# Kernel tuning notes

Measured on AMD Instinct MI355X. Metric: run time of the kernel, lower is better.

## Reference

```python
import jax, jax.numpy as jnp
import numpy as np

N_USERS = 100000
N_ITEMS = 100000
N_NODES = N_USERS + N_ITEMS
NNZ = 3200000
EMB = 64
HOPS = 3


def setup_inputs() -> dict:
    key = jax.random.key(0)
    ks = jax.random.split(key, 9)
    return {
        "rows": jax.random.randint(ks[0], (NNZ,), 0, N_NODES, dtype=jnp.int32),
        "cols": jax.random.randint(ks[1], (NNZ,), 0, N_NODES, dtype=jnp.int32),
        "vals": jax.random.uniform(ks[2], (NNZ,), dtype=jnp.float32),
        "user_emb": jax.random.normal(ks[3], (N_USERS, EMB), dtype=jnp.float32) * 0.1,
        "item_emb": jax.random.normal(ks[4], (N_ITEMS, EMB), dtype=jnp.float32) * 0.1,
        "W_gc": jax.random.normal(ks[5], (HOPS, EMB, EMB), dtype=jnp.float32) * 0.1,
        "b_gc": jax.random.normal(ks[6], (HOPS, EMB), dtype=jnp.float32) * 0.1,
        "W_bi": jax.random.normal(ks[7], (HOPS, EMB, EMB), dtype=jnp.float32) * 0.1,
        "b_bi": jax.random.normal(ks[8], (HOPS, EMB), dtype=jnp.float32) * 0.1,
    }


def reference(rows, cols, vals, user_emb, item_emb, W_gc, b_gc, W_bi, b_bi):
    # NGCF.gcn with edge_dropout=False, mess_dropout=False.
    n_nodes = user_emb.shape[0] + item_emb.shape[0]
    ego = jnp.concatenate([user_emb, item_emb], axis=0)  # [N, d]
    all_embeddings = [ego]
    for k in range(W_gc.shape[0]):
        # sparse adjacency propagation: side = A_hat @ ego
        msgs = vals[:, None] * ego[cols]                       # [nnz, d]
        side = jax.ops.segment_sum(msgs, rows, num_segments=n_nodes)  # [N, d]
        sum_emb = side @ W_gc[k] + b_gc[k]                     # [N, d]
        bi_emb = (ego * side) @ W_bi[k] + b_bi[k]              # [N, d]
        ego = jax.nn.leaky_relu(sum_emb + bi_emb, negative_slope=0.2)
        nrm = jnp.sqrt(jnp.sum(ego * ego, axis=1, keepdims=True))
        all_embeddings.append(ego / jnp.maximum(nrm, 1e-12))   # F.normalize(p=2, dim=1)
    # [N, hops+1, d]; original splits into users/items — concatenated here
    return jnp.stack(all_embeddings, axis=1)
```

## Files before the change

kernel.cpp:

```cpp
#include <hip/hip_runtime.h>
#include <hip/hip_fp16.h>

#define N_USERS 100000
#define N_ITEMS 100000
#define N_NODES 200000
#define NNZ     3200000
#define EMB     64
#define HOPS    3
#define SLOTS   (HOPS + 1)
#define ROWSTRIDE (SLOTS * EMB)

#define BROWS 1024
#define NBUCK ((N_NODES + BROWS - 1) / BROWS)
#define CAPB  20
#define EPB   2048
#define TILE  64
#define LPAD  33


__global__ __launch_bounds__(256) void init_ego_q(
    const float* __restrict__ user_emb,
    const float* __restrict__ item_emb,
    float* __restrict__ out,
    signed char* __restrict__ ego8, float* __restrict__ esc)
{
    int gid = blockIdx.x * blockDim.x + threadIdx.x;
    int n = gid >> 6;
    int d = gid & 63;
    if (n >= N_NODES) return;
    float v = (n < N_USERS) ? user_emb[(size_t)n * EMB + d]
                            : item_emb[(size_t)(n - N_USERS) * EMB + d];
    out[(size_t)n * ROWSTRIDE + d] = v;

    float mx = fabsf(v);
    #pragma unroll
    for (int o = 32; o > 0; o >>= 1) mx = fmaxf(mx, __shfl_xor(mx, o));
    float inv = (mx > 0.f) ? 127.f / mx : 0.f;
    ego8[(size_t)n * EMB + d] = (signed char)__float2int_rn(v * inv);
    if (d == 0) esc[n] = mx * (1.f / 127.f);
}

__global__ __launch_bounds__(256) void hist_buckets(
    const int* __restrict__ rows, int* __restrict__ bcnt)
{
    __shared__ int h[NBUCK];
    int t = threadIdx.x;
    if (t < NBUCK) h[t] = 0;
    __syncthreads();
    for (int e = blockIdx.x * blockDim.x + t; e < NNZ; e += gridDim.x * blockDim.x)
        atomicAdd(&h[rows[e] >> 10], 1);
    __syncthreads();
    if (t < NBUCK && h[t]) atomicAdd(&bcnt[t], h[t]);
}

__global__ __launch_bounds__(256) void scan196(
    const int* __restrict__ bcnt, int* __restrict__ boff,
    int* __restrict__ gcur, int* __restrict__ off)
{
    __shared__ int sdata[256];
    int t = threadIdx.x;
    int v = (t < NBUCK) ? bcnt[t] : 0;
    sdata[t] = v;
    __syncthreads();
    #pragma unroll
    for (int ofs = 1; ofs < 256; ofs <<= 1) {
        int add = (t >= ofs) ? sdata[t - ofs] : 0;
        __syncthreads();
        sdata[t] += add;
        __syncthreads();
    }
    if (t < NBUCK) {
        int excl = sdata[t] - v;
        boff[t] = excl;
        gcur[t] = excl;
    }
    if (t == NBUCK - 1) boff[NBUCK] = sdata[t];
    if (t == 0) off[N_NODES] = NNZ;
}

__global__ __launch_bounds__(256) void bucketize(
    const int* __restrict__ rows, const int* __restrict__ cols,
    const float* __restrict__ vals,
    int* __restrict__ gcur,
    unsigned int* __restrict__ cvg, unsigned short* __restrict__ rlg)
{
    __shared__ int hist[NBUCK];
    __shared__ int lofs[NBUCK];
    __shared__ int cnt2[NBUCK];
    __shared__ int gbase[NBUCK];
    __shared__ int sscan[256];
    __shared__ unsigned int   stcv[EPB];
    __shared__ unsigned short strl[EPB];
    __shared__ int            sdst[EPB];

    int t = threadIdx.x;

    for (int base = blockIdx.x * EPB; base < NNZ; base += gridDim.x * EPB) {
        int e1 = min(base + EPB, NNZ);
        int cnt = e1 - base;

        if (t < NBUCK) { hist[t] = 0; cnt2[t] = 0; }
        __syncthreads();

        int myb[8];
        unsigned int mycv[8];
        unsigned short myrl[8];
        #pragma unroll
        for (int u = 0; u < 8; ++u) {
            int idx = base + u * 256 + t;
            myb[u] = -1;
            if (idx < e1) {
                int r = rows[idx];
                int c = cols[idx];
                float v = vals[idx];
                myb[u] = r >> 10;
                unsigned int q14 = (unsigned int)(v * 16383.f + 0.5f);
                mycv[u] = ((unsigned int)c << 14) | q14;
                myrl[u] = (unsigned short)(r & 1023);
                atomicAdd(&hist[myb[u]], 1);
            }
        }
        __syncthreads();

        int hv = (t < NBUCK) ? hist[t] : 0;
        sscan[t] = hv;
        __syncthreads();
        #pragma unroll
        for (int o = 1; o < 256; o <<= 1) {
            int add = (t >= o) ? sscan[t - o] : 0;
            __syncthreads();
            sscan[t] += add;
            __syncthreads();
        }
        if (t < NBUCK) {
            lofs[t] = sscan[t] - hv;
            gbase[t] = atomicAdd(&gcur[t], hv);
        }
        __syncthreads();

        #pragma unroll
        for (int u = 0; u < 8; ++u) {
            if (myb[u] >= 0) {
                int rank = atomicAdd(&cnt2[myb[u]], 1);
                int p = lofs[myb[u]] + rank;
                stcv[p] = mycv[u];
                strl[p] = myrl[u];
                sdst[p] = gbase[myb[u]] + rank;
            }
        }
        __syncthreads();

        for (int j = t; j < cnt; j += 256) {
            int dp = sdst[j];
            cvg[dp] = stcv[j];
            rlg[dp] = strl[j];
        }
        __syncthreads();
    }
}

__global__ __launch_bounds__(1024) void csr_bucket(
    const int* __restrict__ boff,
    unsigned int* __restrict__ cv, const unsigned short* __restrict__ rl,
    int* __restrict__ off)
{
    __shared__ int curL[BROWS];
    __shared__ int sWaveSum[16];
    __shared__ int sWaveOff[16];

    int b = blockIdx.x;
    int t = threadIdx.x;
    int s = boff[b];
    int e = boff[b + 1];

    unsigned int  ecv[CAPB];
    unsigned short erl[CAPB];
    #pragma unroll
    for (int i = 0; i < CAPB; ++i) {
        int idx = s + i * 1024 + t;
        if (idx < e) { ecv[i] = cv[idx]; erl[i] = rl[idx]; }
    }

    curL[t] = 0;
    __syncthreads();

    #pragma unroll
    for (int i = 0; i < CAPB; ++i) {
        int idx = s + i * 1024 + t;
        if (idx < e) atomicAdd(&curL[(int)erl[i]], 1);
    }
    __syncthreads();

    int lane = t & 63;
    int wid  = t >> 6;
    int v = curL[t];
    int inc = v;
    #pragma unroll
    for (int o = 1; o < 64; o <<= 1) {
        int up = __shfl_up(inc, o);
        if (lane >= o) inc += up;
    }
    if (lane == 63) sWaveSum[wid] = inc;
    __syncthreads();
    if (t < 16) {
        int w = sWaveSum[t];
        int wi = w;
        #pragma unroll
        for (int o = 1; o < 16; o <<= 1) {
            int up = __shfl_up(wi, o);
            if (t >= o) wi += up;
        }
        sWaveOff[t] = wi - w;
    }
    __syncthreads();
    int excl = inc - v + sWaveOff[wid];

    int row = b * BROWS + t;
    if (row < N_NODES) off[row] = s + excl;
    __syncthreads();
    curL[t] = s + excl;
    __syncthreads();

    #pragma unroll
    for (int i = 0; i < CAPB; ++i) {
        int idx = s + i * 1024 + t;
        if (idx < e) {
            int p = atomicAdd(&curL[(int)erl[i]], 1);
            cv[p] = ecv[i];
        }
    }
}

__global__ __launch_bounds__(256) void scale_edges(
    const uint4* __restrict__ cv4, const float* __restrict__ esc,
    ushort4* __restrict__ wn4)
{
    const float VS = 1.f / 16383.f;
    int i = blockIdx.x * blockDim.x + threadIdx.x;
    if (i >= NNZ / 4) return;
    uint4 c = cv4[i];
    ushort4 w;
    w.x = __half_as_ushort(__float2half((float)(c.x & 16383u) * VS * esc[c.x >> 14]));
    w.y = __half_as_ushort(__float2half((float)(c.y & 16383u) * VS * esc[c.y >> 14]));
    w.z = __half_as_ushort(__float2half((float)(c.z & 16383u) * VS * esc[c.z >> 14]));
    w.w = __half_as_ushort(__float2half((float)(c.w & 16383u) * VS * esc[c.w >> 14]));
    wn4[i] = w;
}

__device__ __forceinline__ void gstep4(
    const signed char* __restrict__ ego8,
    unsigned c0, unsigned c1, unsigned c2, unsigned c3,
    unsigned wlo, unsigned whi, unsigned g, unsigned dq,
    float& a0, float& a1, float& a2, float& a3)
{
    unsigned cs = (g & 2u) ? ((g & 1u) ? c3 : c2) : ((g & 1u) ? c1 : c0);
    unsigned wd = (g & 2u) ? whi : wlo;
    unsigned short wh = (g & 1u) ? (unsigned short)(wd >> 16)
                                 : (unsigned short)(wd & 0xFFFFu);
    float w = __half2float(__ushort_as_half(wh));
    uchar4 x4 = *(const uchar4*)(ego8 + (size_t)(cs >> 14) * EMB + dq * 4u);
    a0 = fmaf(w, (float)(signed char)x4.x, a0);
    a1 = fmaf(w, (float)(signed char)x4.y, a1);
    a2 = fmaf(w, (float)(signed char)x4.z, a2);
    a3 = fmaf(w, (float)(signed char)x4.w, a3);
}

__device__ __forceinline__ void gstepm(
    const signed char* __restrict__ ego8,
    const unsigned int* __restrict__ cv, const unsigned short* __restrict__ wn,
    int e, int hi, unsigned g, unsigned dq,
    float& a0, float& a1, float& a2, float& a3)
{
    int idx = e + (int)g;
    int cl = (idx < hi) ? idx : hi - 1;
    unsigned c = cv[cl];
    float w = (idx < hi) ? __half2float(__ushort_as_half(wn[cl])) : 0.f;
    uchar4 x4 = *(const uchar4*)(ego8 + (size_t)(c >> 14) * EMB + dq * 4u);
    a0 = fmaf(w, (float)(signed char)x4.x, a0);
    a1 = fmaf(w, (float)(signed char)x4.y, a1);
    a2 = fmaf(w, (float)(signed char)x4.z, a2);
    a3 = fmaf(w, (float)(signed char)x4.w, a3);
}

__global__ __launch_bounds__(256, 4) void gather_side(
    const int* __restrict__ off, const unsigned int* __restrict__ cv,
    const unsigned short* __restrict__ wn,
    const signed char* __restrict__ ego8,
    float* __restrict__ out, int k)
{
    int t = threadIdx.x;
    int lane = t & 63;
    unsigned g  = (unsigned)(lane >> 4);
    unsigned dq = (unsigned)(lane & 15);
    int gw = (int)((blockIdx.x * (size_t)blockDim.x + t) >> 6);
    int nw = (gridDim.x * blockDim.x) >> 6;

    float* dst = out + (size_t)(k + 1) * EMB;

    for (int n = gw; n < N_NODES; n += nw) {
        int beg = __builtin_amdgcn_readfirstlane(off[n]);
        int end = __builtin_amdgcn_readfirstlane(off[n + 1]);
        float a0 = 0.f, a1 = 0.f, a2 = 0.f, a3 = 0.f;
        int e = beg;
        if (e < end && (e & 3)) {
            int ea = (e + 3) & ~3;
            int ub = (ea < end) ? ea : end;
            gstepm(ego8, cv, wn, e, ub, g, dq, a0, a1, a2, a3);
            e = ea;
        }
        for (; e + 16 <= end; e += 16) {
            uint4 ca = *(const uint4*)(cv + e);
            uint4 cb = *(const uint4*)(cv + e + 4);
            uint4 cc = *(const uint4*)(cv + e + 8);
            uint4 cd = *(const uint4*)(cv + e + 12);
            uint2 w0 = *(const uint2*)(wn + e);
            uint2 w1 = *(const uint2*)(wn + e + 4);
            uint2 w2 = *(const uint2*)(wn + e + 8);
            uint2 w3 = *(const uint2*)(wn + e + 12);
            gstep4(ego8, ca.x, ca.y, ca.z, ca.w, w0.x, w0.y, g, dq, a0, a1, a2, a3);
            gstep4(ego8, cb.x, cb.y, cb.z, cb.w, w1.x, w1.y, g, dq, a0, a1, a2, a3);
            gstep4(ego8, cc.x, cc.y, cc.z, cc.w, w2.x, w2.y, g, dq, a0, a1, a2, a3);
            gstep4(ego8, cd.x, cd.y, cd.z, cd.w, w3.x, w3.y, g, dq, a0, a1, a2, a3);
        }
        for (; e < end; e += 4)
            gstepm(ego8, cv, wn, e, end, g, dq, a0, a1, a2, a3);

        a0 += __shfl_xor(a0, 16); a0 += __shfl_xor(a0, 32);
        a1 += __shfl_xor(a1, 16); a1 += __shfl_xor(a1, 32);
        a2 += __shfl_xor(a2, 16); a2 += __shfl_xor(a2, 32);
        a3 += __shfl_xor(a3, 16); a3 += __shfl_xor(a3, 32);
        if (g == 0) {
            float4 o4; o4.x = a0; o4.y = a1; o4.z = a2; o4.w = a3;
            *(float4*)(dst + (size_t)n * ROWSTRIDE + dq * 4u) = o4;
        }
    }
}

__global__ __launch_bounds__(256) void transform_v4(
    const float* __restrict__ Wg, const float* __restrict__ bg,
    const float* __restrict__ Wb, const float* __restrict__ bb,
    signed char* __restrict__ ego8, float* __restrict__ esc,
    float* __restrict__ out, int k, int writeNext)
{
    __shared__ float sS [TILE * LPAD];
    __shared__ float sES[TILE * LPAD];
    __shared__ float rsum[4][TILE];
    __shared__ float rmax[4][TILE];

    int t = threadIdx.x;
    int lane = t & 63;
    int dbase = __builtin_amdgcn_readfirstlane((t >> 6) * 16);

    float* slotK1 = out + (size_t)(k + 1) * EMB;
    int node0 = blockIdx.x * TILE;

    float acc[16];
    #pragma unroll
    for (int di = 0; di < 16; ++di) acc[di] = 0.f;

    int f4 = (t & 7) * 4;
    int nn = t >> 3;

    for (int p = 0; p < 2; ++p) {
        #pragma unroll
        for (int rep = 0; rep < 2; ++rep) {
            int n = nn + 32 * rep;
            size_t sbase = (size_t)(node0 + n) * ROWSTRIDE + 32 * p + f4;
            float4 s4 = *(const float4*)(slotK1 + sbase);
            uchar4 e4 = *(const uchar4*)(ego8 + (size_t)(node0 + n) * EMB + 32 * p + f4);
            float scn = esc[node0 + n];
            int lb = n * LPAD + f4;
            sS [lb + 0] = s4.x; sS [lb + 1] = s4.y; sS [lb + 2] = s4.z; sS [lb + 3] = s4.w;
            sES[lb + 0] = (float)(signed char)e4.x * scn * s4.x;
            sES[lb + 1] = (float)(signed char)e4.y * scn * s4.y;
            sES[lb + 2] = (float)(signed char)e4.z * scn * s4.z;
            sES[lb + 3] = (float)(signed char)e4.w * scn * s4.w;
        }
        __syncthreads();

        for (int jj = 0; jj < 32; ++jj) {
            float sv = sS [lane * LPAD + jj];
            float ev = sES[lane * LPAD + jj];
            int j = 32 * p + jj;
            const float* wgrow = Wg + j * EMB + dbase;
            const float* wbrow = Wb + j * EMB + dbase;
            #pragma unroll
            for (int di = 0; di < 16; ++di)
                acc[di] = fmaf(sv, wgrow[di], fmaf(ev, wbrow[di], acc[di]));
        }
        __syncthreads();
    }

    float o[16];
    float ps = 0.f, pm = 0.f;
    #pragma unroll
    for (int di = 0; di < 16; ++di) {
        float v = acc[di] + (bg[dbase + di] + bb[dbase + di]);
        v = (v > 0.f) ? v : 0.2f * v;
        o[di] = v;
        ps = fmaf(v, v, ps);
        pm = fmaxf(pm, fabsf(v));
    }
    int w = t >> 6;
    rsum[w][lane] = ps;
    rmax[w][lane] = pm;
    __syncthreads();
    float tot = rsum[0][lane] + rsum[1][lane] + rsum[2][lane] + rsum[3][lane];
    float mx  = fmaxf(fmaxf(rmax[0][lane], rmax[1][lane]),
                      fmaxf(rmax[2][lane], rmax[3][lane]));
    float scale = 1.f / fmaxf(sqrtf(tot), 1e-12f);

    if (writeNext) {
        float inv = (mx > 0.f) ? 127.f / mx : 0.f;
        unsigned int wd[4];
        #pragma unroll
        for (int q = 0; q < 4; ++q) {
            unsigned int b0 = (unsigned int)(unsigned char)(signed char)__float2int_rn(o[4*q+0] * inv);
            unsigned int b1 = (unsigned int)(unsigned char)(signed char)__float2int_rn(o[4*q+1] * inv);
            unsigned int b2 = (unsigned int)(unsigned char)(signed char)__float2int_rn(o[4*q+2] * inv);
            unsigned int b3 = (unsigned int)(unsigned char)(signed char)__float2int_rn(o[4*q+3] * inv);
            wd[q] = b0 | (b1 << 8) | (b2 << 16) | (b3 << 24);
        }
        uint4 pk; pk.x = wd[0]; pk.y = wd[1]; pk.z = wd[2]; pk.w = wd[3];
        *(uint4*)(ego8 + (size_t)(node0 + lane) * EMB + dbase) = pk;
        if (t < TILE) esc[node0 + lane] = mx * (1.f / 127.f);
    }

    float* dstp = slotK1 + (size_t)(node0 + lane) * ROWSTRIDE + dbase;
    #pragma unroll
    for (int q = 0; q < 4; ++q) {
        float4 o4;
        o4.x = o[4 * q + 0] * scale;
        o4.y = o[4 * q + 1] * scale;
        o4.z = o[4 * q + 2] * scale;
        o4.w = o[4 * q + 3] * scale;
        *(float4*)(dstp + 4 * q) = o4;
    }
}

extern "C" void kernel_launch(void* const* d_in, const int* in_sizes, int n_in,
                              void* d_out, int out_size, void* d_ws, size_t ws_size,
                              hipStream_t stream)
{
    const int*   rows     = (const int*)d_in[0];
    const int*   cols     = (const int*)d_in[1];
    const float* vals     = (const float*)d_in[2];
    const float* user_emb = (const float*)d_in[3];
    const float* item_emb = (const float*)d_in[4];
    const float* W_gc     = (const float*)d_in[5];
    const float* b_gc     = (const float*)d_in[6];
    const float* W_bi     = (const float*)d_in[7];
    const float* b_bi     = (const float*)d_in[8];
    float* out = (float*)d_out;

    signed char* ego8 = (signed char*)d_ws;
    float* esc = (float*)(ego8 + (size_t)N_NODES * EMB);
    int* bcnt = (int*)(esc + N_NODES);
    int* boff = bcnt + NBUCK;
    int* gcur = boff + NBUCK + 1;
    int* off  = gcur + NBUCK;
    unsigned int* cv = (unsigned int*)(off + N_NODES + 1 + 2);
    unsigned short* wn = (unsigned short*)(cv + NNZ);
    unsigned short* rl = wn + NNZ;

    hipMemsetAsync(bcnt, 0, NBUCK * sizeof(int), stream);
    hist_buckets<<<1024, 256, 0, stream>>>(rows, bcnt);
    scan196<<<1, 256, 0, stream>>>(bcnt, boff, gcur, off);
    bucketize<<<512, 256, 0, stream>>>(rows, cols, vals, gcur, cv, rl);
    csr_bucket<<<NBUCK, 1024, 0, stream>>>(boff, cv, rl, off);

    init_ego_q<<<(N_NODES * 64) / 256, 256, 0, stream>>>(
        user_emb, item_emb, out, ego8, esc);

    scale_edges<<<(NNZ / 4 + 255) / 256, 256, 0, stream>>>(
        (const uint4*)cv, esc, (ushort4*)wn);

    for (int k = 0; k < HOPS; ++k) {
        gather_side<<<2048, 256, 0, stream>>>(off, cv, wn, ego8, out, k);
        transform_v4<<<N_NODES / TILE, 256, 0, stream>>>(
            W_gc + (size_t)k * EMB * EMB, b_gc + (size_t)k * EMB,
            W_bi + (size_t)k * EMB * EMB, b_bi + (size_t)k * EMB,
            ego8, esc, out, k, (k < HOPS - 1) ? 1 : 0);
        if (k < HOPS - 1)
            scale_edges<<<(NNZ / 4 + 255) / 256, 256, 0, stream>>>(
                (const uint4*)cv, esc, (ushort4*)wn);
    }
}
```

Baseline: 657.0 us.

## Fuse sparse gather and dense transform into one per-hop kernel with ping-pong ego buffers

Merges the gather (SpMM) and transform kernels into a single hop kernel. Each block gathers side rows for 64 nodes straight into shared memory and then does the transform, so the side embedding no longer round-trips through global memory. Because blocks now read the old quantized ego while others write the new one, ego8/esc are double-buffered and swapped between hops. This also drops the grid-stride warp scheduling in the gather, which may cost load balance and occupancy (launch_bounds min-blocks hint removed, larger LDS). The histogram kernel is also vectorized to int4 loads with half the blocks.

```diff
diff --git a/kernel.cpp b/kernel.cpp
--- a/kernel.cpp
+++ b/kernel.cpp
@@ -15,7 +15,7 @@
 #define CAPB  20
 #define EPB   2048
 #define TILE  64
-#define LPAD  33
+#define SPAD  65
 
 
 __global__ __launch_bounds__(256) void init_ego_q(
@@ -41,14 +41,19 @@
 }
 
 __global__ __launch_bounds__(256) void hist_buckets(
-    const int* __restrict__ rows, int* __restrict__ bcnt)
+    const int4* __restrict__ rows4, int* __restrict__ bcnt)
 {
     __shared__ int h[NBUCK];
     int t = threadIdx.x;
     if (t < NBUCK) h[t] = 0;
     __syncthreads();
-    for (int e = blockIdx.x * blockDim.x + t; e < NNZ; e += gridDim.x * blockDim.x)
-        atomicAdd(&h[rows[e] >> 10], 1);
+    for (int i = blockIdx.x * blockDim.x + t; i < NNZ / 4; i += gridDim.x * blockDim.x) {
+        int4 r = rows4[i];
+        atomicAdd(&h[r.x >> 10], 1);
+        atomicAdd(&h[r.y >> 10], 1);
+        atomicAdd(&h[r.z >> 10], 1);
+        atomicAdd(&h[r.w >> 10], 1);
+    }
     __syncthreads();
     if (t < NBUCK && h[t]) atomicAdd(&bcnt[t], h[t]);
 }
@@ -282,22 +287,30 @@
     a3 = fmaf(w, (float)(signed char)x4.w, a3);
 }
 
-__global__ __launch_bounds__(256, 4) void gather_side(
+__global__ __launch_bounds__(256) void hop_fused(
     const int* __restrict__ off, const unsigned int* __restrict__ cv,
     const unsigned short* __restrict__ wn,
-    const signed char* __restrict__ ego8,
-    float* __restrict__ out, int k)
-{
+    const signed char* __restrict__ egoIn, const float* __restrict__ escIn,
+    signed char* __restrict__ egoOut, float* __restrict__ escOut,
+    const float* __restrict__ Wg, const float* __restrict__ bg,
+    const float* __restrict__ Wb, const float* __restrict__ bb,
+    float* __restrict__ out, int k, int writeNext)
+{
+    __shared__ float sS [TILE * SPAD];
+    __shared__ float sES[TILE * SPAD];
+    __shared__ float rsum[4][TILE];
+    __shared__ float rmax[4][TILE];
+
     int t = threadIdx.x;
     int lane = t & 63;
+    int w = t >> 6;
     unsigned g  = (unsigned)(lane >> 4);
     unsigned dq = (unsigned)(lane & 15);
-    int gw = (int)((blockIdx.x * (size_t)blockDim.x + t) >> 6);
-    int nw = (gridDim.x * blockDim.x) >> 6;
-
-    float* dst = out + (size_t)(k + 1) * EMB;
-
-    for (int n = gw; n < N_NODES; n += nw) {
+    int node0 = blockIdx.x * TILE;
+
+    for (int i = 0; i < 16; ++i) {
+        int ln = w * 16 + i;
+        int n = node0 + ln;
         int beg = __builtin_amdgcn_readfirstlane(off[n]);
         int end = __builtin_amdgcn_readfirstlane(off[n + 1]);
         float a0 = 0.f, a1 = 0.f, a2 = 0.f, a3 = 0.f;
@@ -305,7 +318,7 @@
         if (e < end && (e & 3)) {
             int ea = (e + 3) & ~3;
             int ub = (ea < end) ? ea : end;
-            gstepm(ego8, cv, wn, e, ub, g, dq, a0, a1, a2, a3);
+            gstepm(egoIn, cv, wn, e, ub, g, dq, a0, a1, a2, a3);
             e = ea;
         }
         for (; e + 16 <= end; e += 16) {
@@ -317,78 +330,56 @@
             uint2 w1 = *(const uint2*)(wn + e + 4);
             uint2 w2 = *(const uint2*)(wn + e + 8);
             uint2 w3 = *(const uint2*)(wn + e + 12);
-            gstep4(ego8, ca.x, ca.y, ca.z, ca.w, w0.x, w0.y, g, dq, a0, a1, a2, a3);
-            gstep4(ego8, cb.x, cb.y, cb.z, cb.w, w1.x, w1.y, g, dq, a0, a1, a2, a3);
-            gstep4(ego8, cc.x, cc.y, cc.z, cc.w, w2.x, w2.y, g, dq, a0, a1, a2, a3);
-            gstep4(ego8, cd.x, cd.y, cd.z, cd.w, w3.x, w3.y, g, dq, a0, a1, a2, a3);
+            gstep4(egoIn, ca.x, ca.y, ca.z, ca.w, w0.x, w0.y, g, dq, a0, a1, a2, a3);
+            gstep4(egoIn, cb.x, cb.y, cb.z, cb.w, w1.x, w1.y, g, dq, a0, a1, a2, a3);
+            gstep4(egoIn, cc.x, cc.y, cc.z, cc.w, w2.x, w2.y, g, dq, a0, a1, a2, a3);
+            gstep4(egoIn, cd.x, cd.y, cd.z, cd.w, w3.x, w3.y, g, dq, a0, a1, a2, a3);
         }
         for (; e < end; e += 4)
-            gstepm(ego8, cv, wn, e, end, g, dq, a0, a1, a2, a3);
+            gstepm(egoIn, cv, wn, e, end, g, dq, a0, a1, a2, a3);
 
         a0 += __shfl_xor(a0, 16); a0 += __shfl_xor(a0, 32);
         a1 += __shfl_xor(a1, 16); a1 += __shfl_xor(a1, 32);
         a2 += __shfl_xor(a2, 16); a2 += __shfl_xor(a2, 32);
         a3 += __shfl_xor(a3, 16); a3 += __shfl_xor(a3, 32);
         if (g == 0) {
-            float4 o4; o4.x = a0; o4.y = a1; o4.z = a2; o4.w = a3;
-            *(float4*)(dst + (size_t)n * ROWSTRIDE + dq * 4u) = o4;
-        }
-    }
-}
-
-__global__ __launch_bounds__(256) void transform_v4(
-    const float* __restrict__ Wg, const float* __restrict__ bg,
-    const float* __restrict__ Wb, const float* __restrict__ bb,
-    signed char* __restrict__ ego8, float* __restrict__ esc,
-    float* __restrict__ out, int k, int writeNext)
-{
-    __shared__ float sS [TILE * LPAD];
-    __shared__ float sES[TILE * LPAD];
-    __shared__ float rsum[4][TILE];
-    __shared__ float rmax[4][TILE];
-
-    int t = threadIdx.x;
-    int lane = t & 63;
-    int dbase = __builtin_amdgcn_readfirstlane((t >> 6) * 16);
-
-    float* slotK1 = out + (size_t)(k + 1) * EMB;
-    int node0 = blockIdx.x * TILE;
-
+            int lb = ln * SPAD + (int)dq * 4;
+            sS[lb + 0] = a0; sS[lb + 1] = a1; sS[lb + 2] = a2; sS[lb + 3] = a3;
+        }
+    }
+    __syncthreads();
+
+    {
+        int nn = t >> 2;
+        int f16 = (t & 3) * 16;
+        float scn = escIn[node0 + nn];
+        uint4 eb = *(const uint4*)(egoIn + (size_t)(node0 + nn) * EMB + f16);
+        int lb = nn * SPAD + f16;
+        unsigned wds[4] = { eb.x, eb.y, eb.z, eb.w };
+        #pragma unroll
+        for (int q = 0; q < 4; ++q) {
+            #pragma unroll
+            for (int b = 0; b < 4; ++b) {
+                float ev = (float)(signed char)((wds[q] >> (8 * b)) & 0xFFu);
+                sES[lb + q * 4 + b] = ev * scn * sS[lb + q * 4 + b];
+            }
+        }
+    }
+    __syncthreads();
+
+    int dbase = __builtin_amdgcn_readfirstlane(w * 16);
     float acc[16];
     #pragma unroll
     for (int di = 0; di < 16; ++di) acc[di] = 0.f;
 
-    int f4 = (t & 7) * 4;
-    int nn = t >> 3;
-
-    for (int p = 0; p < 2; ++p) {
-        #pragma unroll
-        for (int rep = 0; rep < 2; ++rep) {
-            int n = nn + 32 * rep;
-            size_t sbase = (size_t)(node0 + n) * ROWSTRIDE + 32 * p + f4;
-            float4 s4 = *(const float4*)(slotK1 + sbase);
-            uchar4 e4 = *(const uchar4*)(ego8 + (size_t)(node0 + n) * EMB + 32 * p + f4);
-            float scn = esc[node0 + n];
-            int lb = n * LPAD + f4;
-            sS [lb + 0] = s4.x; sS [lb + 1] = s4.y; sS [lb + 2] = s4.z; sS [lb + 3] = s4.w;
-            sES[lb + 0] = (float)(signed char)e4.x * scn * s4.x;
-            sES[lb + 1] = (float)(signed char)e4.y * scn * s4.y;
-            sES[lb + 2] = (float)(signed char)e4.z * scn * s4.z;
-            sES[lb + 3] = (float)(signed char)e4.w * scn * s4.w;
-        }
-        __syncthreads();
-
-        for (int jj = 0; jj < 32; ++jj) {
-            float sv = sS [lane * LPAD + jj];
-            float ev = sES[lane * LPAD + jj];
-            int j = 32 * p + jj;
-            const float* wgrow = Wg + j * EMB + dbase;
-            const float* wbrow = Wb + j * EMB + dbase;
-            #pragma unroll
-            for (int di = 0; di < 16; ++di)
-                acc[di] = fmaf(sv, wgrow[di], fmaf(ev, wbrow[di], acc[di]));
-        }
-        __syncthreads();
+    for (int j = 0; j < 64; ++j) {
+        float sv = sS [lane * SPAD + j];
+        float ev = sES[lane * SPAD + j];
+        const float* wgrow = Wg + j * EMB + dbase;
+        const float* wbrow = Wb + j * EMB + dbase;
+        #pragma unroll
+        for (int di = 0; di < 16; ++di)
+            acc[di] = fmaf(sv, wgrow[di], fmaf(ev, wbrow[di], acc[di]));
     }
 
     float o[16];
@@ -401,7 +392,6 @@
         ps = fmaf(v, v, ps);
         pm = fmaxf(pm, fabsf(v));
     }
-    int w = t >> 6;
     rsum[w][lane] = ps;
     rmax[w][lane] = pm;
     __syncthreads();
@@ -422,11 +412,11 @@
             wd[q] = b0 | (b1 << 8) | (b2 << 16) | (b3 << 24);
         }
         uint4 pk; pk.x = wd[0]; pk.y = wd[1]; pk.z = wd[2]; pk.w = wd[3];
-        *(uint4*)(ego8 + (size_t)(node0 + lane) * EMB + dbase) = pk;
-        if (t < TILE) esc[node0 + lane] = mx * (1.f / 127.f);
-    }
-
-    float* dstp = slotK1 + (size_t)(node0 + lane) * ROWSTRIDE + dbase;
+        *(uint4*)(egoOut + (size_t)(node0 + lane) * EMB + dbase) = pk;
+        if (t < TILE) escOut[node0 + lane] = mx * (1.f / 127.f);
+    }
+
+    float* dstp = out + (size_t)(node0 + lane) * ROWSTRIDE + (size_t)(k + 1) * EMB + dbase;
     #pragma unroll
     for (int q = 0; q < 4; ++q) {
         float4 o4;
@@ -453,9 +443,11 @@
     const float* b_bi     = (const float*)d_in[8];
     float* out = (float*)d_out;
 
-    signed char* ego8 = (signed char*)d_ws;
-    float* esc = (float*)(ego8 + (size_t)N_NODES * EMB);
-    int* bcnt = (int*)(esc + N_NODES);
+    signed char* ego8A = (signed char*)d_ws;
+    signed char* ego8B = ego8A + (size_t)N_NODES * EMB;
+    float* escA = (float*)(ego8B + (size_t)N_NODES * EMB);
+    float* escB = escA + N_NODES;
+    int* bcnt = (int*)(escB + N_NODES);
     int* boff = bcnt + NBUCK;
     int* gcur = boff + NBUCK + 1;
     int* off  = gcur + NBUCK;
@@ -464,25 +456,32 @@
     unsigned short* rl = wn + NNZ;
 
     hipMemsetAsync(bcnt, 0, NBUCK * sizeof(int), stream);
-    hist_buckets<<<1024, 256, 0, stream>>>(rows, bcnt);
+    hist_buckets<<<512, 256, 0, stream>>>((const int4*)rows, bcnt);
     scan196<<<1, 256, 0, stream>>>(bcnt, boff, gcur, off);
     bucketize<<<512, 256, 0, stream>>>(rows, cols, vals, gcur, cv, rl);
     csr_bucket<<<NBUCK, 1024, 0, stream>>>(boff, cv, rl, off);
 
     init_ego_q<<<(N_NODES * 64) / 256, 256, 0, stream>>>(
-        user_emb, item_emb, out, ego8, esc);
+        user_emb, item_emb, out, ego8A, escA);
 
     scale_edges<<<(NNZ / 4 + 255) / 256, 256, 0, stream>>>(
-        (const uint4*)cv, esc, (ushort4*)wn);
-
+        (const uint4*)cv, escA, (ushort4*)wn);
+
+    const signed char* eIn = ego8A;
+    signed char*       eOut = ego8B;
+    const float*       sIn = escA;
+    float*             sOut = escB;
     for (int k = 0; k < HOPS; ++k) {
-        gather_side<<<2048, 256, 0, stream>>>(off, cv, wn, ego8, out, k);
-        transform_v4<<<N_NODES / TILE, 256, 0, stream>>>(
+        hop_fused<<<N_NODES / TILE, 256, 0, stream>>>(
+            off, cv, wn, eIn, sIn, eOut, sOut,
             W_gc + (size_t)k * EMB * EMB, b_gc + (size_t)k * EMB,
             W_bi + (size_t)k * EMB * EMB, b_bi + (size_t)k * EMB,
-            ego8, esc, out, k, (k < HOPS - 1) ? 1 : 0);
-        if (k < HOPS - 1)
+            out, k, (k < HOPS - 1) ? 1 : 0);
+        if (k < HOPS - 1) {
             scale_edges<<<(NNZ / 4 + 255) / 256, 256, 0, stream>>>(
-                (const uint4*)cv, esc, (ushort4*)wn);
-    }
-}
+                (const uint4*)cv, sOut, (ushort4*)wn);
+            const signed char* tIn = eIn; eIn = eOut; eOut = (signed char*)tIn;
+            const float* tS = sIn; sIn = sOut; sOut = (float*)tS;
+        }
+    }
+}
```

After: 885.1 us. +34.7%, slower.

## Process two CSR rows per wavefront in gather and vectorize histogram loads

Applied to the files above, without the earlier changes.

The gather kernel now has each wavefront handle two consecutive nodes as one contiguous edge range. Edges are routed to one of two accumulator sets by comparing against the midpoint offset. This amortizes per-row overhead and partial-group waste for low-degree rows (average degree 16), at the cost of doubling accumulators and the FMA count per edge. Separately, the bucket histogram reads rows as int4 with half as many blocks to reduce load instruction count.

```diff
diff --git a/kernel.cpp b/kernel.cpp
--- a/kernel.cpp
+++ b/kernel.cpp
@@ -41,14 +41,19 @@
 }
 
 __global__ __launch_bounds__(256) void hist_buckets(
-    const int* __restrict__ rows, int* __restrict__ bcnt)
+    const int4* __restrict__ rows4, int* __restrict__ bcnt)
 {
     __shared__ int h[NBUCK];
     int t = threadIdx.x;
     if (t < NBUCK) h[t] = 0;
     __syncthreads();
-    for (int e = blockIdx.x * blockDim.x + t; e < NNZ; e += gridDim.x * blockDim.x)
-        atomicAdd(&h[rows[e] >> 10], 1);
+    for (int i = blockIdx.x * blockDim.x + t; i < NNZ / 4; i += gridDim.x * blockDim.x) {
+        int4 r = rows4[i];
+        atomicAdd(&h[r.x >> 10], 1);
+        atomicAdd(&h[r.y >> 10], 1);
+        atomicAdd(&h[r.z >> 10], 1);
+        atomicAdd(&h[r.w >> 10], 1);
+    }
     __syncthreads();
     if (t < NBUCK && h[t]) atomicAdd(&bcnt[t], h[t]);
 }
@@ -247,39 +252,56 @@
     wn4[i] = w;
 }
 
-__device__ __forceinline__ void gstep4(
+__device__ __forceinline__ void gstep4d(
     const signed char* __restrict__ ego8,
     unsigned c0, unsigned c1, unsigned c2, unsigned c3,
     unsigned wlo, unsigned whi, unsigned g, unsigned dq,
-    float& a0, float& a1, float& a2, float& a3)
+    int ebase, int mid,
+    float& a0, float& a1, float& a2, float& a3,
+    float& b0, float& b1, float& b2, float& b3)
 {
     unsigned cs = (g & 2u) ? ((g & 1u) ? c3 : c2) : ((g & 1u) ? c1 : c0);
     unsigned wd = (g & 2u) ? whi : wlo;
     unsigned short wh = (g & 1u) ? (unsigned short)(wd >> 16)
                                  : (unsigned short)(wd & 0xFFFFu);
     float w = __half2float(__ushort_as_half(wh));
+    bool toA = (ebase + (int)g) < mid;
+    float wa = toA ? w : 0.f;
+    float wb = toA ? 0.f : w;
     uchar4 x4 = *(const uchar4*)(ego8 + (size_t)(cs >> 14) * EMB + dq * 4u);
-    a0 = fmaf(w, (float)(signed char)x4.x, a0);
-    a1 = fmaf(w, (float)(signed char)x4.y, a1);
-    a2 = fmaf(w, (float)(signed char)x4.z, a2);
-    a3 = fmaf(w, (float)(signed char)x4.w, a3);
-}
-
-__device__ __forceinline__ void gstepm(
+    float x0 = (float)(signed char)x4.x;
+    float x1 = (float)(signed char)x4.y;
+    float x2 = (float)(signed char)x4.z;
+    float x3 = (float)(signed char)x4.w;
+    a0 = fmaf(wa, x0, a0); b0 = fmaf(wb, x0, b0);
+    a1 = fmaf(wa, x1, a1); b1 = fmaf(wb, x1, b1);
+    a2 = fmaf(wa, x2, a2); b2 = fmaf(wb, x2, b2);
+    a3 = fmaf(wa, x3, a3); b3 = fmaf(wb, x3, b3);
+}
+
+__device__ __forceinline__ void gstepmd(
     const signed char* __restrict__ ego8,
     const unsigned int* __restrict__ cv, const unsigned short* __restrict__ wn,
-    int e, int hi, unsigned g, unsigned dq,
-    float& a0, float& a1, float& a2, float& a3)
+    int e, int hi, int mid, unsigned g, unsigned dq,
+    float& a0, float& a1, float& a2, float& a3,
+    float& b0, float& b1, float& b2, float& b3)
 {
     int idx = e + (int)g;
     int cl = (idx < hi) ? idx : hi - 1;
     unsigned c = cv[cl];
     float w = (idx < hi) ? __half2float(__ushort_as_half(wn[cl])) : 0.f;
+    bool toA = idx < mid;
+    float wa = toA ? w : 0.f;
+    float wb = toA ? 0.f : w;
     uchar4 x4 = *(const uchar4*)(ego8 + (size_t)(c >> 14) * EMB + dq * 4u);
-    a0 = fmaf(w, (float)(signed char)x4.x, a0);
-    a1 = fmaf(w, (float)(signed char)x4.y, a1);
-    a2 = fmaf(w, (float)(signed char)x4.z, a2);
-    a3 = fmaf(w, (float)(signed char)x4.w, a3);
+    float x0 = (float)(signed char)x4.x;
+    float x1 = (float)(signed char)x4.y;
+    float x2 = (float)(signed char)x4.z;
+    float x3 = (float)(signed char)x4.w;
+    a0 = fmaf(wa, x0, a0); b0 = fmaf(wb, x0, b0);
+    a1 = fmaf(wa, x1, a1); b1 = fmaf(wb, x1, b1);
+    a2 = fmaf(wa, x2, a2); b2 = fmaf(wb, x2, b2);
+    a3 = fmaf(wa, x3, a3); b3 = fmaf(wb, x3, b3);
 }
 
 __global__ __launch_bounds__(256, 4) void gather_side(
@@ -297,17 +319,20 @@
 
     float* dst = out + (size_t)(k + 1) * EMB;
 
-    for (int n = gw; n < N_NODES; n += nw) {
+    for (int n = gw * 2; n < N_NODES; n += nw * 2) {
         int beg = __builtin_amdgcn_readfirstlane(off[n]);
-        int end = __builtin_amdgcn_readfirstlane(off[n + 1]);
+        int mid = __builtin_amdgcn_readfirstlane(off[n + 1]);
+        int end = __builtin_amdgcn_readfirstlane(off[n + 2]);
         float a0 = 0.f, a1 = 0.f, a2 = 0.f, a3 = 0.f;
+        float b0 = 0.f, b1 = 0.f, b2 = 0.f, b3 = 0.f;
         int e = beg;
         if (e < end && (e & 3)) {
             int ea = (e + 3) & ~3;
             int ub = (ea < end) ? ea : end;
-            gstepm(ego8, cv, wn, e, ub, g, dq, a0, a1, a2, a3);
+            gstepmd(ego8, cv, wn, e, ub, mid, g, dq, a0, a1, a2, a3, b0, b1, b2, b3);
             e = ea;
         }
+        #pragma unroll 2
         for (; e + 16 <= end; e += 16) {
             uint4 ca = *(const uint4*)(cv + e);
             uint4 cb = *(const uint4*)(cv + e + 4);
@@ -317,21 +342,27 @@
             uint2 w1 = *(const uint2*)(wn + e + 4);
             uint2 w2 = *(const uint2*)(wn + e + 8);
             uint2 w3 = *(const uint2*)(wn + e + 12);
-            gstep4(ego8, ca.x, ca.y, ca.z, ca.w, w0.x, w0.y, g, dq, a0, a1, a2, a3);
-            gstep4(ego8, cb.x, cb.y, cb.z, cb.w, w1.x, w1.y, g, dq, a0, a1, a2, a3);
-            gstep4(ego8, cc.x, cc.y, cc.z, cc.w, w2.x, w2.y, g, dq, a0, a1, a2, a3);
-            gstep4(ego8, cd.x, cd.y, cd.z, cd.w, w3.x, w3.y, g, dq, a0, a1, a2, a3);
+            gstep4d(ego8, ca.x, ca.y, ca.z, ca.w, w0.x, w0.y, g, dq, e,      mid, a0, a1, a2, a3, b0, b1, b2, b3);
+            gstep4d(ego8, cb.x, cb.y, cb.z, cb.w, w1.x, w1.y, g, dq, e + 4,  mid, a0, a1, a2, a3, b0, b1, b2, b3);
+            gstep4d(ego8, cc.x, cc.y, cc.z, cc.w, w2.x, w2.y, g, dq, e + 8,  mid, a0, a1, a2, a3, b0, b1, b2, b3);
+            gstep4d(ego8, cd.x, cd.y, cd.z, cd.w, w3.x, w3.y, g, dq, e + 12, mid, a0, a1, a2, a3, b0, b1, b2, b3);
         }
         for (; e < end; e += 4)
-            gstepm(ego8, cv, wn, e, end, g, dq, a0, a1, a2, a3);
+            gstepmd(ego8, cv, wn, e, end, mid, g, dq, a0, a1, a2, a3, b0, b1, b2, b3);
 
         a0 += __shfl_xor(a0, 16); a0 += __shfl_xor(a0, 32);
         a1 += __shfl_xor(a1, 16); a1 += __shfl_xor(a1, 32);
         a2 += __shfl_xor(a2, 16); a2 += __shfl_xor(a2, 32);
         a3 += __shfl_xor(a3, 16); a3 += __shfl_xor(a3, 32);
+        b0 += __shfl_xor(b0, 16); b0 += __shfl_xor(b0, 32);
+        b1 += __shfl_xor(b1, 16); b1 += __shfl_xor(b1, 32);
+        b2 += __shfl_xor(b2, 16); b2 += __shfl_xor(b2, 32);
+        b3 += __shfl_xor(b3, 16); b3 += __shfl_xor(b3, 32);
         if (g == 0) {
             float4 o4; o4.x = a0; o4.y = a1; o4.z = a2; o4.w = a3;
             *(float4*)(dst + (size_t)n * ROWSTRIDE + dq * 4u) = o4;
+            float4 p4; p4.x = b0; p4.y = b1; p4.z = b2; p4.w = b3;
+            *(float4*)(dst + (size_t)(n + 1) * ROWSTRIDE + dq * 4u) = p4;
         }
     }
 }
@@ -464,7 +495,7 @@
     unsigned short* rl = wn + NNZ;
 
     hipMemsetAsync(bcnt, 0, NBUCK * sizeof(int), stream);
-    hist_buckets<<<1024, 256, 0, stream>>>(rows, bcnt);
+    hist_buckets<<<512, 256, 0, stream>>>((const int4*)rows, bcnt);
     scan196<<<1, 256, 0, stream>>>(bcnt, boff, gcur, off);
     bucketize<<<512, 256, 0, stream>>>(rows, cols, vals, gcur, cv, rl);
     csr_bucket<<<NBUCK, 1024, 0, stream>>>(boff, cv, rl, off);
```

Measured after the change: 593.0 us. 9.7% less time.
